# Kernel optimization log

Hardware: AMD Instinct MI355X
Metric: run time of the kernel (lower is better)

The kernel has to match this reference:

```python
import jax, jax.numpy as jnp
import numpy as np

GRID_NUM = 3  # pykan 'grid' (number of intervals)
K = 3         # spline order

def bspline_basis(x, grid, k):
    # Cox-de Boor recursion, matching pykan B_batch with a shared extended grid.
    # x: (N, Din); grid: (G,) extended grid with G = GRID_NUM + 2*k + 1
    x = x[..., None]  # (N, Din, 1)
    B = ((x >= grid[:-1]) & (x < grid[1:])).astype(x.dtype)  # (N, Din, G-1)
    for p in range(1, k + 1):
        left = (x - grid[:-(p + 1)]) / (grid[p:-1] - grid[:-(p + 1)])
        right = (grid[p + 1:] - x) / (grid[p + 1:] - grid[1:-p])
        B = left * B[..., :-1] + right * B[..., 1:]
    return B  # (N, Din, GRID_NUM + k)

def setup_inputs() -> dict:
    key = jax.random.key(0)
    k1, k2, k3 = jax.random.split(key, 3)
    Bsz, S, Din, Dout = 4, 2048, 768, 768
    x = jax.random.normal(k1, (Bsz, S, Din), dtype=jnp.float32)
    # noise-scale-like init for spline coefficients (noise_scale=0.1)
    coef = (0.1 / GRID_NUM) * jax.random.normal(k2, (Dout, Din, GRID_NUM + K), dtype=jnp.float32)
    inv_sqrt_in = np.float32(1.0 / np.sqrt(Din))
    scale_base = inv_sqrt_in + 0.1 * inv_sqrt_in * jax.random.normal(k3, (Dout, Din), dtype=jnp.float32)
    scale_sp = jnp.ones((Dout, Din), dtype=jnp.float32)
    bias = jnp.zeros((Dout,), dtype=jnp.float32)
    return {"x": x, "coef": coef, "scale_base": scale_base, "scale_sp": scale_sp, "bias": bias}

def reference(x, coef, scale_base, scale_sp, bias):
    # x: (B, S, Din) -> flatten tokens as the original module does
    Bsz, S, Din = x.shape
    xf = x.reshape(-1, Din)  # (N, Din)
    # extended grid: linspace(-1,1,GRID_NUM+1) extended by K points each side (h = 2/GRID_NUM)
    h = 2.0 / GRID_NUM
    grid = jnp.arange(-K, GRID_NUM + K + 1, dtype=x.dtype) * h - 1.0  # (GRID_NUM + 2K + 1,)
    basis = bspline_basis(xf, grid, K)  # (N, Din, GRID_NUM+K)
    # per-edge activation: scale_base*silu(x) + scale_sp*spline(x); mask==1; symbolic branch==0
    base = jax.nn.silu(xf) @ scale_base.T  # (N, Dout)
    spline = jnp.einsum('nim,oim->no', basis, scale_sp[:, :, None] * coef)  # (N, Dout)
    out = base + spline + bias  # bias from pykan biases[l].weight
    return out.reshape(Bsz, S, -1)
```

## Files before the change

kernel.cpp:

```cpp
#include <hip/hip_runtime.h>
#include <hip/hip_bf16.h>


typedef _Float16 f16;
typedef __attribute__((ext_vector_type(8))) _Float16 f16x8;
typedef __attribute__((ext_vector_type(4))) float f32x4;

#define NTOK 8192
#define DIN 768
#define DOUT 768
#define KAUG 5376
#define BM 128
#define BN 128
#define BK 32
#define KT (KAUG / BK)

typedef __attribute__((address_space(1))) void gvoid;
typedef __attribute__((address_space(3))) void lvoid;

__global__ __launch_bounds__(256) void build_A(const float* __restrict__ x,
                                               f16* __restrict__ Aa) {
  int idx = blockIdx.x * 256 + threadIdx.x;
  float xv = x[idx];
  int n = idx / DIN;
  int i = idx - n * DIN;

  float s = xv / (1.0f + __expf(-xv));

  const float h = 2.0f / 3.0f;
  float B[9];
#pragma unroll
  for (int g = 0; g < 9; ++g) {
    float t0 = (float)(g - 3) * h - 1.0f;
    float t1 = (float)(g - 2) * h - 1.0f;
    B[g] = (xv >= t0 && xv < t1) ? 1.0f : 0.0f;
  }
#pragma unroll
  for (int p = 1; p <= 3; ++p) {
    float inv = 1.0f / ((float)p * h);
#pragma unroll
    for (int j = 0; j < 9 - 3; ++j) {
      if (j < 9 - p) {
        float tj = (float)(j - 3) * h - 1.0f;
        float tjp1 = (float)(j + p + 1 - 3) * h - 1.0f;
        B[j] = (xv - tj) * inv * B[j] + (tjp1 - xv) * inv * B[j + 1];
      }
    }
#pragma unroll
    for (int j = 6; j < 9; ++j) {
      if (j < 9 - p) {
        float tj = (float)(j - 3) * h - 1.0f;
        float tjp1 = (float)(j + p + 1 - 3) * h - 1.0f;
        B[j] = (xv - tj) * inv * B[j] + (tjp1 - xv) * inv * B[j + 1];
      }
    }
  }

  size_t base = (size_t)n * KAUG + i;
  Aa[base] = (f16)s;
#pragma unroll
  for (int m = 0; m < 6; ++m) Aa[base + (size_t)(m + 1) * DIN] = (f16)B[m];
}

__global__ __launch_bounds__(256) void build_W(const float* __restrict__ sb,
                                               const float* __restrict__ ssp,
                                               const float* __restrict__ coef,
                                               f16* __restrict__ Wa) {
  int idx = blockIdx.x * 256 + threadIdx.x;
  float b = sb[idx];
  float sp = ssp[idx];
  int o = idx / DIN;
  int i = idx - o * DIN;
  size_t base = (size_t)o * KAUG + i;
  Wa[base] = (f16)b;
#pragma unroll
  for (int m = 0; m < 6; ++m)
    Wa[base + (size_t)(m + 1) * DIN] = (f16)(sp * coef[(size_t)idx * 6 + m]);
}

__global__ __launch_bounds__(256) void kan_gemm(const f16* __restrict__ A,
                                                const f16* __restrict__ W,
                                                const float* __restrict__ bias,
                                                float* __restrict__ out) {
  __shared__ alignas(16) f16 As[BM * BK];
  __shared__ alignas(16) f16 Bs[BN * BK];

  const int tid = threadIdx.x;
  const int wave = tid >> 6;
  const int lane = tid & 63;
  const int m0 = blockIdx.y * BM;
  const int n0 = blockIdx.x * BN;
  const int wm = (wave >> 1) * 64;
  const int wn = (wave & 1) * 64;
  const int r = lane & 15;
  const int q = lane >> 4;

  f32x4 acc[4][4] = {};

  const int c0 = wave * 64 + lane;
  const int rowA0 = c0 >> 2, kb0 = c0 & 3;
  const int c1 = c0 + 256;
  const int rowA1 = c1 >> 2, kb1 = c1 & 3;

  const f16* gA0 = A + (size_t)(m0 + rowA0) * KAUG + kb0 * 8;
  const f16* gA1 = A + (size_t)(m0 + rowA1) * KAUG + kb1 * 8;
  const f16* gB0 = W + (size_t)(n0 + rowA0) * KAUG + kb0 * 8;
  const f16* gB1 = W + (size_t)(n0 + rowA1) * KAUG + kb1 * 8;

  f16* ldsA = As + wave * 512;
  f16* ldsB = Bs + wave * 512;

  for (int kt = 0; kt < KT; ++kt) {
    const int koff = kt * BK;
    __builtin_amdgcn_global_load_lds((gvoid*)(gA0 + koff), (lvoid*)(ldsA), 16, 0, 0);
    __builtin_amdgcn_global_load_lds((gvoid*)(gA1 + koff), (lvoid*)(ldsA + 2048), 16, 0, 0);
    __builtin_amdgcn_global_load_lds((gvoid*)(gB0 + koff), (lvoid*)(ldsB), 16, 0, 0);
    __builtin_amdgcn_global_load_lds((gvoid*)(gB1 + koff), (lvoid*)(ldsB + 2048), 16, 0, 0);
    __syncthreads();

    f16x8 af[4], bf[4];
#pragma unroll
    for (int mi = 0; mi < 4; ++mi)
      af[mi] = *(const f16x8*)&As[(wm + mi * 16 + r) * BK + q * 8];
#pragma unroll
    for (int ni = 0; ni < 4; ++ni)
      bf[ni] = *(const f16x8*)&Bs[(wn + ni * 16 + r) * BK + q * 8];
#pragma unroll
    for (int mi = 0; mi < 4; ++mi)
#pragma unroll
      for (int ni = 0; ni < 4; ++ni)
        acc[mi][ni] =
            __builtin_amdgcn_mfma_f32_16x16x32_f16(af[mi], bf[ni], acc[mi][ni], 0, 0, 0);
    __syncthreads();
  }

#pragma unroll
  for (int mi = 0; mi < 4; ++mi) {
#pragma unroll
    for (int ni = 0; ni < 4; ++ni) {
      const int gcol = n0 + wn + ni * 16 + r;
      const float bv = bias[gcol];
#pragma unroll
      for (int rg = 0; rg < 4; ++rg) {
        const int grow = m0 + wm + mi * 16 + q * 4 + rg;
        out[(size_t)grow * DOUT + gcol] = acc[mi][ni][rg] + bv;
      }
    }
  }
}

extern "C" void kernel_launch(void* const* d_in, const int* in_sizes, int n_in,
                              void* d_out, int out_size, void* d_ws, size_t ws_size,
                              hipStream_t stream) {
  const float* x = (const float*)d_in[0];
  const float* coef = (const float*)d_in[1];
  const float* scale_base = (const float*)d_in[2];
  const float* scale_sp = (const float*)d_in[3];
  const float* bias = (const float*)d_in[4];
  float* out = (float*)d_out;

  f16* Aa = (f16*)d_ws;
  f16* Wa = (f16*)((char*)d_ws + (size_t)NTOK * KAUG * 2);

  build_A<<<(NTOK * DIN) / 256, 256, 0, stream>>>(x, Aa);
  build_W<<<(DOUT * DIN) / 256, 256, 0, stream>>>(scale_base, scale_sp, coef, Wa);
  kan_gemm<<<dim3(DOUT / BN, NTOK / BM), 256, 0, stream>>>(Aa, Wa, bias, out);
}
```

Before: 225.2 us.

## Vectorize basis build, double-buffer GEMM LDS, and remap blocks per XCD

build_A now handles 8 inputs per thread, loading with float4 and storing with f16x8. It evaluates the uniform cubic B-spline in closed form from the fractional grid position instead of running the Cox-de Boor recursion. The GEMM double-buffers its LDS tiles so the next K-slice loads while MFMAs run on the current one, which drops one barrier per iteration. It also remaps the 1D block index so that blocks landing on the same XCD share A row tiles, which should improve L2 reuse. Risks: half-open boundary handling in the closed-form basis may differ slightly from the reference, and LDS use doubles.

```diff
diff --git a/kernel.cpp b/kernel.cpp
--- a/kernel.cpp
+++ b/kernel.cpp
@@ -20,46 +20,43 @@
 
 __global__ __launch_bounds__(256) void build_A(const float* __restrict__ x,
                                                f16* __restrict__ Aa) {
-  int idx = blockIdx.x * 256 + threadIdx.x;
-  float xv = x[idx];
-  int n = idx / DIN;
-  int i = idx - n * DIN;
+  const int t = blockIdx.x * 256 + threadIdx.x;
+  const int n = t / 96;
+  const int i8 = (t - n * 96) * 8;
 
-  float s = xv / (1.0f + __expf(-xv));
+  const float4* xp = (const float4*)(x + (size_t)n * DIN + i8);
+  float4 va = xp[0], vb = xp[1];
+  float xv[8] = {va.x, va.y, va.z, va.w, vb.x, vb.y, vb.z, vb.w};
 
-  const float h = 2.0f / 3.0f;
-  float B[9];
+  f16x8 sil;
+  f16x8 Bv[6];
 #pragma unroll
-  for (int g = 0; g < 9; ++g) {
-    float t0 = (float)(g - 3) * h - 1.0f;
-    float t1 = (float)(g - 2) * h - 1.0f;
-    B[g] = (xv >= t0 && xv < t1) ? 1.0f : 0.0f;
-  }
+  for (int e = 0; e < 8; ++e) {
+    const float v = xv[e];
+    sil[e] = (f16)__fdividef(v, 1.0f + __expf(-v));
+
+    const float s = (v + 1.0f) * 1.5f + 3.0f;
+    const float fi = floorf(s);
+    const int i0 = (int)fi;
+    const float u = s - fi;
+    const float um = 1.0f - u;
+    const float u2 = u * u, u3 = u2 * u;
+    const float w0 = um * um * um * (1.0f / 6.0f);
+    const float w1 = (3.0f * u3 - 6.0f * u2 + 4.0f) * (1.0f / 6.0f);
+    const float w2 = (-3.0f * u3 + 3.0f * u2 + 3.0f * u + 1.0f) * (1.0f / 6.0f);
+    const float w3 = u3 * (1.0f / 6.0f);
 #pragma unroll
-  for (int p = 1; p <= 3; ++p) {
-    float inv = 1.0f / ((float)p * h);
-#pragma unroll
-    for (int j = 0; j < 9 - 3; ++j) {
-      if (j < 9 - p) {
-        float tj = (float)(j - 3) * h - 1.0f;
-        float tjp1 = (float)(j + p + 1 - 3) * h - 1.0f;
-        B[j] = (xv - tj) * inv * B[j] + (tjp1 - xv) * inv * B[j + 1];
-      }
-    }
-#pragma unroll
-    for (int j = 6; j < 9; ++j) {
-      if (j < 9 - p) {
-        float tj = (float)(j - 3) * h - 1.0f;
-        float tjp1 = (float)(j + p + 1 - 3) * h - 1.0f;
-        B[j] = (xv - tj) * inv * B[j] + (tjp1 - xv) * inv * B[j + 1];
-      }
+    for (int m = 0; m < 6; ++m) {
+      const int d = m - i0 + 3;
+      float w = (d == 0) ? w0 : (d == 1) ? w1 : (d == 2) ? w2 : (d == 3) ? w3 : 0.0f;
+      Bv[m][e] = (f16)w;
     }
   }
 
-  size_t base = (size_t)n * KAUG + i;
-  Aa[base] = (f16)s;
+  const size_t base = (size_t)n * KAUG + i8;
+  *(f16x8*)&Aa[base] = sil;
 #pragma unroll
-  for (int m = 0; m < 6; ++m) Aa[base + (size_t)(m + 1) * DIN] = (f16)B[m];
+  for (int m = 0; m < 6; ++m) *(f16x8*)&Aa[base + (size_t)(m + 1) * DIN] = Bv[m];
 }
 
 __global__ __launch_bounds__(256) void build_W(const float* __restrict__ sb,
@@ -82,14 +79,20 @@
                                                 const f16* __restrict__ W,
                                                 const float* __restrict__ bias,
                                                 float* __restrict__ out) {
-  __shared__ alignas(16) f16 As[BM * BK];
-  __shared__ alignas(16) f16 Bs[BN * BK];
+  __shared__ alignas(16) f16 As[2][BM * BK];
+  __shared__ alignas(16) f16 Bs[2][BN * BK];
+
+  const int bid = blockIdx.x;
+  const int xcd = bid & 7;
+  const int slot = bid >> 3;
+  const int mb = ((slot & 7) << 3) + xcd;
+  const int nb = slot >> 3;
+  const int m0 = mb * BM;
+  const int n0 = nb * BN;
 
   const int tid = threadIdx.x;
   const int wave = tid >> 6;
   const int lane = tid & 63;
-  const int m0 = blockIdx.y * BM;
-  const int n0 = blockIdx.x * BN;
   const int wm = (wave >> 1) * 64;
   const int wn = (wave & 1) * 64;
   const int r = lane & 15;
@@ -107,39 +110,44 @@
   const f16* gB0 = W + (size_t)(n0 + rowA0) * KAUG + kb0 * 8;
   const f16* gB1 = W + (size_t)(n0 + rowA1) * KAUG + kb1 * 8;
 
-  f16* ldsA = As + wave * 512;
-  f16* ldsB = Bs + wave * 512;
+  const int woff = wave * 512;
+
+  auto stage = [&](int buf, int kt) {
+    const int koff = kt * BK;
+    __builtin_amdgcn_global_load_lds((gvoid*)(gA0 + koff), (lvoid*)(&As[buf][woff]), 16, 0, 0);
+    __builtin_amdgcn_global_load_lds((gvoid*)(gA1 + koff), (lvoid*)(&As[buf][woff + 2048]), 16, 0, 0);
+    __builtin_amdgcn_global_load_lds((gvoid*)(gB0 + koff), (lvoid*)(&Bs[buf][woff]), 16, 0, 0);
+    __builtin_amdgcn_global_load_lds((gvoid*)(gB1 + koff), (lvoid*)(&Bs[buf][woff + 2048]), 16, 0, 0);
+  };
+
+  stage(0, 0);
 
   for (int kt = 0; kt < KT; ++kt) {
-    const int koff = kt * BK;
-    __builtin_amdgcn_global_load_lds((gvoid*)(gA0 + koff), (lvoid*)(ldsA), 16, 0, 0);
-    __builtin_amdgcn_global_load_lds((gvoid*)(gA1 + koff), (lvoid*)(ldsA + 2048), 16, 0, 0);
-    __builtin_amdgcn_global_load_lds((gvoid*)(gB0 + koff), (lvoid*)(ldsB), 16, 0, 0);
-    __builtin_amdgcn_global_load_lds((gvoid*)(gB1 + koff), (lvoid*)(ldsB + 2048), 16, 0, 0);
+    const int buf = kt & 1;
     __syncthreads();
+    if (kt + 1 < KT) stage(buf ^ 1, kt + 1);
 
     f16x8 af[4], bf[4];
 #pragma unroll
     for (int mi = 0; mi < 4; ++mi)
-      af[mi] = *(const f16x8*)&As[(wm + mi * 16 + r) * BK + q * 8];
+      af[mi] = *(const f16x8*)&As[buf][(wm + mi * 16 + r) * BK + q * 8];
 #pragma unroll
     for (int ni = 0; ni < 4; ++ni)
-      bf[ni] = *(const f16x8*)&Bs[(wn + ni * 16 + r) * BK + q * 8];
+      bf[ni] = *(const f16x8*)&Bs[buf][(wn + ni * 16 + r) * BK + q * 8];
 #pragma unroll
     for (int mi = 0; mi < 4; ++mi)
 #pragma unroll
       for (int ni = 0; ni < 4; ++ni)
         acc[mi][ni] =
             __builtin_amdgcn_mfma_f32_16x16x32_f16(af[mi], bf[ni], acc[mi][ni], 0, 0, 0);
-    __syncthreads();
   }
 
 #pragma unroll
-  for (int mi = 0; mi < 4; ++mi) {
+  for (int ni = 0; ni < 4; ++ni) {
+    const int gcol = n0 + wn + ni * 16 + r;
+    const float bv = bias[gcol];
 #pragma unroll
-    for (int ni = 0; ni < 4; ++ni) {
-      const int gcol = n0 + wn + ni * 16 + r;
-      const float bv = bias[gcol];
+    for (int mi = 0; mi < 4; ++mi) {
 #pragma unroll
       for (int rg = 0; rg < 4; ++rg) {
         const int grow = m0 + wm + mi * 16 + q * 4 + rg;
@@ -162,7 +170,7 @@
   f16* Aa = (f16*)d_ws;
   f16* Wa = (f16*)((char*)d_ws + (size_t)NTOK * KAUG * 2);
 
-  build_A<<<(NTOK * DIN) / 256, 256, 0, stream>>>(x, Aa);
+  build_A<<<(NTOK * DIN / 8) / 256, 256, 0, stream>>>(x, Aa);
   build_W<<<(DOUT * DIN) / 256, 256, 0, stream>>>(scale_base, scale_sp, coef, Wa);
-  kan_gemm<<<dim3(DOUT / BN, NTOK / BM), 256, 0, stream>>>(Aa, Wa, bias, out);
+  kan_gemm<<<6 * 64, 256, 0, stream>>>(Aa, Wa, bias, out);
 }
```

After: 239.2 us. 6.2% more time.
